# Kernel tuning notes

Hardware: AMD Instinct MI355X
Metric: run time of the kernel (lower is better)

## Reference

```python
import jax, jax.numpy as jnp
import numpy as np

HQ = 32      # query heads
HKV = 8      # kv heads
DH = 128     # head dim
B, S, D = 8, 1, 4096
MAX_SEQ = 4096


def rope(x, pos):
    """Rotary embedding on interleaved pairs. x: [B,S,H,dh], pos: [S] int."""
    d = x.shape[-1]
    theta = 1.0 / (10000.0 ** (jnp.arange(0, d, 2, dtype=jnp.float32) / d))  # [d/2]
    ang = pos[:, None].astype(jnp.float32) * theta[None, :]                  # [S,d/2]
    cos = jnp.cos(ang)[None, :, None, :]
    sin = jnp.sin(ang)[None, :, None, :]
    xr, xi = x[..., 0::2], x[..., 1::2]
    out_r = xr * cos - xi * sin
    out_i = xr * sin + xi * cos
    return jnp.stack([out_r, out_i], axis=-1).reshape(x.shape)


def setup_inputs() -> dict:
    key = jax.random.key(0)
    ks = jax.random.split(key, 8)
    s = 0.02
    return {
        "x": jax.random.normal(ks[0], (B, S, D), jnp.float32),
        "wq": jax.random.normal(ks[1], (D, HQ * DH), jnp.float32) * s,
        "bq": jnp.zeros((HQ * DH,), jnp.float32),
        "wk": jax.random.normal(ks[2], (D, HKV * DH), jnp.float32) * s,
        "bk": jnp.zeros((HKV * DH,), jnp.float32),
        "wv": jax.random.normal(ks[3], (D, HKV * DH), jnp.float32) * s,
        "bv": jnp.zeros((HKV * DH,), jnp.float32),
        "wo": jax.random.normal(ks[4], (HQ * DH, D), jnp.float32) * s,
        "bo": jnp.zeros((D,), jnp.float32),
        "cache_k": jax.random.normal(ks[5], (B, MAX_SEQ, HKV, DH), jnp.float32) * 0.5,
        "cache_v": jax.random.normal(ks[6], (B, MAX_SEQ, HKV, DH), jnp.float32) * 0.5,
        "start_pos": MAX_SEQ - S,  # decode step at end of cache
    }


def reference(x, wq, bq, wk, bk, wv, bv, wo, bo, cache_k, cache_v, start_pos):
    b, s, d = x.shape
    n_rep = HQ // HKV
    q = (x @ wq + bq).reshape(b, s, HQ, DH)
    k = (x @ wk + bk).reshape(b, s, HKV, DH)
    v = (x @ wv + bv).reshape(b, s, HKV, DH)
    pos = start_pos + jnp.arange(s)
    q = rope(q, pos)
    k = rope(k, pos)
    # KV-cache scatter write
    cache_k = jax.lax.dynamic_update_slice(cache_k, k, (0, start_pos, 0, 0))
    cache_v = jax.lax.dynamic_update_slice(cache_v, v, (0, start_pos, 0, 0))
    t = start_pos + s  # static (start_pos is a Python int)
    keys = cache_k[:, :t]    # [B,T,HKV,DH]
    values = cache_v[:, :t]
    # repeat_kv: duplicate each kv head n_rep times -> [B,T,HQ,DH]
    keys = jnp.repeat(keys, n_rep, axis=2)
    values = jnp.repeat(values, n_rep, axis=2)
    # naive softmax attention, score matrix materialized
    scores = jnp.einsum("bshd,bthd->bhst", q, keys) * (DH ** -0.5)  # [B,HQ,S,T]
    attn = jax.nn.softmax(scores, axis=-1)
    out = jnp.einsum("bhst,bthd->bshd", attn, values).reshape(b, s, HQ * DH)
    return out @ wo + bo
```

## Files before the change

### kernel.cpp

```cpp
#include <hip/hip_runtime.h>
#include <cmath>

#define NB 8
#define DIM 4096
#define NHQ 32
#define NHKV 8
#define NDH 128
#define MAXSEQ 4096
#define STARTPOS 4095
#define QKV_COLS 6144
#define RCHUNK 64
#define NRC 64
#define SCALE 0.08838834764831845f

__global__ __launch_bounds__(256) void qkv_partial_k(
    const float* __restrict__ x, const float* __restrict__ wq,
    const float* __restrict__ wk, const float* __restrict__ wv,
    float* __restrict__ part) {
  int bid = blockIdx.x;
  int ct = bid % 12, rc = bid / 12;
  int tid = threadIdx.x;
  const float* W; int ldw; int colbase;
  int gcolbase = ct * 512;
  if (ct < 8)       { W = wq; ldw = NHQ * NDH;  colbase = gcolbase; }
  else if (ct < 10) { W = wk; ldw = NHKV * NDH; colbase = gcolbase - 4096; }
  else              { W = wv; ldw = NHKV * NDH; colbase = gcolbase - 5120; }

  __shared__ __align__(16) float xs[RCHUNK][8];
  int rbase = rc * RCHUNK;
  for (int i = tid; i < RCHUNK * 8; i += 256) {
    int b = i >> 6, r = i & 63;
    xs[r][b] = x[b * DIM + rbase + r];
  }
  __syncthreads();

  int col = colbase + tid * 2;
  const float* wp = W + (size_t)rbase * ldw + col;
  float2 acc[8];
#pragma unroll
  for (int b = 0; b < 8; b++) { acc[b].x = 0.f; acc[b].y = 0.f; }

#pragma unroll 8
  for (int r = 0; r < RCHUNK; r++) {
    float2 w2 = *(const float2*)wp; wp += ldw;
    float4 xa = *(const float4*)&xs[r][0];
    float4 xb = *(const float4*)&xs[r][4];
    acc[0].x += xa.x * w2.x; acc[0].y += xa.x * w2.y;
    acc[1].x += xa.y * w2.x; acc[1].y += xa.y * w2.y;
    acc[2].x += xa.z * w2.x; acc[2].y += xa.z * w2.y;
    acc[3].x += xa.w * w2.x; acc[3].y += xa.w * w2.y;
    acc[4].x += xb.x * w2.x; acc[4].y += xb.x * w2.y;
    acc[5].x += xb.y * w2.x; acc[5].y += xb.y * w2.y;
    acc[6].x += xb.z * w2.x; acc[6].y += xb.z * w2.y;
    acc[7].x += xb.w * w2.x; acc[7].y += xb.w * w2.y;
  }
  int gcol = gcolbase + tid * 2;
#pragma unroll
  for (int b = 0; b < 8; b++)
    *(float2*)&part[((size_t)rc * 8 + b) * QKV_COLS + gcol] = acc[b];
}

__global__ __launch_bounds__(256) void qkv_reduce_rope_k(
    const float* __restrict__ part, const float* __restrict__ bq,
    const float* __restrict__ bk, const float* __restrict__ bv,
    float* __restrict__ qws, float* __restrict__ kws, float* __restrict__ vws) {
  int idx = blockIdx.x * 256 + threadIdx.x;
  int b = idx / QKV_COLS, col = idx % QKV_COLS;
  float s = 0.f;
#pragma unroll 8
  for (int rcc = 0; rcc < NRC; rcc++)
    s += part[((size_t)rcc * 8 + b) * QKV_COLS + col];
  float bias = (col < 4096) ? bq[col] : (col < 5120 ? bk[col - 4096] : bv[col - 5120]);
  s += bias;
  float outv = s;
  if (col < 5120) {
    int dim = col & 127;
    int i2 = dim & ~1;
    float theta = powf(10000.f, -(float)i2 * (1.f / 128.f));
    float ang = (float)STARTPOS * theta;
    float c = cosf(ang), sn = sinf(ang);
    float other = __shfl_xor(s, 1);
    if ((col & 1) == 0) outv = s * c - other * sn;
    else                outv = other * sn + s * c;
  }
  if (col < 4096)       qws[b * 4096 + col] = outv;
  else if (col < 5120)  kws[b * 1024 + (col - 4096)] = outv;
  else                  vws[b * 1024 + (col - 5120)] = outv;
}

__global__ __launch_bounds__(256) void attn_partial_k(
    const float* __restrict__ q, const float* __restrict__ kws,
    const float* __restrict__ vws, const float* __restrict__ ck,
    const float* __restrict__ cv, float* __restrict__ pm,
    float* __restrict__ pl, float* __restrict__ pacc) {
  int bid = blockIdx.x;
  int chunk = bid & 15, grp = bid >> 4;
  int b = grp >> 3, hkv = grp & 7;
  int tid = threadIdx.x;

  __shared__ __align__(16) float kbuf[64][132];
  __shared__ float sbuf[4][256];
  __shared__ __align__(16) float qbuf[4][132];

  for (int i = tid; i < 512; i += 256) {
    int r = i >> 7, d = i & 127;
    qbuf[r][d] = q[b * 4096 + (hkv * 4 + r) * NDH + d];
  }
  __syncthreads();

  int tchunk = chunk * 256;
  int tl_c = tid >> 2;
  int hh = tid & 3;

  for (int tile = 0; tile < 4; tile++) {
    int tbase = tchunk + tile * 64;
#pragma unroll
    for (int i = tid; i < 64 * 32; i += 256) {
      int row = i >> 5, c4 = i & 31;
      int t = tbase + row;
      const float* src = (t == STARTPOS)
          ? (kws + ((size_t)b * NHKV + hkv) * NDH)
          : (ck + (((size_t)b * MAXSEQ + t) * NHKV + hkv) * NDH);
      *(float4*)&kbuf[row][c4 * 4] = *(const float4*)(src + c4 * 4);
    }
    __syncthreads();
    float s0 = 0.f, s1 = 0.f;
    const float4* krow = (const float4*)&kbuf[tl_c][0];
    const float4* qrow = (const float4*)&qbuf[hh][0];
#pragma unroll
    for (int c = 0; c < 32; c += 2) {
      float4 kv = krow[c];     float4 qv = qrow[c];
      s0 += kv.x * qv.x + kv.y * qv.y + kv.z * qv.z + kv.w * qv.w;
      float4 kv2 = krow[c + 1]; float4 qv2 = qrow[c + 1];
      s1 += kv2.x * qv2.x + kv2.y * qv2.y + kv2.z * qv2.z + kv2.w * qv2.w;
    }
    sbuf[hh][tile * 64 + tl_c] = (s0 + s1) * SCALE;
    __syncthreads();
  }

  int wv_ = tid >> 6;
  int lane = tid & 63;
  float e0 = sbuf[wv_][lane];
  float e1 = sbuf[wv_][lane + 64];
  float e2 = sbuf[wv_][lane + 128];
  float e3 = sbuf[wv_][lane + 192];
  float m = fmaxf(fmaxf(e0, e1), fmaxf(e2, e3));
#pragma unroll
  for (int off = 32; off; off >>= 1) m = fmaxf(m, __shfl_xor(m, off));
  float p0 = expf(e0 - m), p1 = expf(e1 - m), p2 = expf(e2 - m), p3 = expf(e3 - m);
  float l = p0 + p1 + p2 + p3;
#pragma unroll
  for (int off = 32; off; off >>= 1) l += __shfl_xor(l, off);
  sbuf[wv_][lane] = p0;
  sbuf[wv_][lane + 64] = p1;
  sbuf[wv_][lane + 128] = p2;
  sbuf[wv_][lane + 192] = p3;
  if (lane == 0) {
    pm[((size_t)grp * 16 + chunk) * 4 + wv_] = m;
    pl[((size_t)grp * 16 + chunk) * 4 + wv_] = l;
  }
  __syncthreads();

  float2 acc2 = {0.f, 0.f};
  int d0 = lane * 2;
  for (int tile = 0; tile < 4; tile++) {
    int tbase = tchunk + tile * 64;
#pragma unroll
    for (int i = tid; i < 64 * 32; i += 256) {
      int row = i >> 5, c4 = i & 31;
      int t = tbase + row;
      const float* src = (t == STARTPOS)
          ? (vws + ((size_t)b * NHKV + hkv) * NDH)
          : (cv + (((size_t)b * MAXSEQ + t) * NHKV + hkv) * NDH);
      *(float4*)&kbuf[row][c4 * 4] = *(const float4*)(src + c4 * 4);
    }
    __syncthreads();
#pragma unroll 8
    for (int tl = 0; tl < 64; tl++) {
      float p = sbuf[wv_][tile * 64 + tl];
      float2 v2 = *(const float2*)&kbuf[tl][d0];
      acc2.x += p * v2.x;
      acc2.y += p * v2.y;
    }
    __syncthreads();
  }
  *(float2*)&pacc[(((size_t)grp * 16 + chunk) * 4 + wv_) * NDH + d0] = acc2;
}

__global__ __launch_bounds__(128) void attn_combine_k(
    const float* __restrict__ pm, const float* __restrict__ pl,
    const float* __restrict__ pacc, float* __restrict__ aout) {
  int bid = blockIdx.x;
  int b = bid >> 5, hq = bid & 31;
  int grp = b * 8 + (hq >> 2), r = hq & 3;
  int d = threadIdx.x;
  float mv[16];
  float M = -1e30f;
#pragma unroll
  for (int c = 0; c < 16; c++) {
    mv[c] = pm[((size_t)grp * 16 + c) * 4 + r];
    M = fmaxf(M, mv[c]);
  }
  float L = 0.f;
  float w[16];
#pragma unroll
  for (int c = 0; c < 16; c++) {
    w[c] = expf(mv[c] - M);
    L += w[c] * pl[((size_t)grp * 16 + c) * 4 + r];
  }
  float o = 0.f;
#pragma unroll
  for (int c = 0; c < 16; c++)
    o += w[c] * pacc[(((size_t)grp * 16 + c) * 4 + r) * NDH + d];
  aout[(size_t)b * 4096 + hq * NDH + d] = o / L;
}

__global__ __launch_bounds__(256) void out_partial_k(
    const float* __restrict__ ain, const float* __restrict__ wo,
    float* __restrict__ part) {
  int bid = blockIdx.x;
  int ct = bid & 7, rc = bid >> 3;
  int tid = threadIdx.x;
  __shared__ __align__(16) float xs[RCHUNK][8];
  int rbase = rc * RCHUNK;
  for (int i = tid; i < RCHUNK * 8; i += 256) {
    int b = i >> 6, r = i & 63;
    xs[r][b] = ain[(size_t)b * 4096 + rbase + r];
  }
  __syncthreads();

  int col = ct * 512 + tid * 2;
  const float* wp = wo + (size_t)rbase * 4096 + col;
  float2 acc[8];
#pragma unroll
  for (int b = 0; b < 8; b++) { acc[b].x = 0.f; acc[b].y = 0.f; }
#pragma unroll 8
  for (int r = 0; r < RCHUNK; r++) {
    float2 w2 = *(const float2*)wp; wp += 4096;
    float4 xa = *(const float4*)&xs[r][0];
    float4 xb = *(const float4*)&xs[r][4];
    acc[0].x += xa.x * w2.x; acc[0].y += xa.x * w2.y;
    acc[1].x += xa.y * w2.x; acc[1].y += xa.y * w2.y;
    acc[2].x += xa.z * w2.x; acc[2].y += xa.z * w2.y;
    acc[3].x += xa.w * w2.x; acc[3].y += xa.w * w2.y;
    acc[4].x += xb.x * w2.x; acc[4].y += xb.x * w2.y;
    acc[5].x += xb.y * w2.x; acc[5].y += xb.y * w2.y;
    acc[6].x += xb.z * w2.x; acc[6].y += xb.z * w2.y;
    acc[7].x += xb.w * w2.x; acc[7].y += xb.w * w2.y;
  }
#pragma unroll
  for (int b = 0; b < 8; b++)
    *(float2*)&part[((size_t)rc * 8 + b) * 4096 + col] = acc[b];
}

__global__ __launch_bounds__(256) void out_reduce_k(
    const float* __restrict__ part, const float* __restrict__ bo,
    float* __restrict__ out) {
  int idx = blockIdx.x * 256 + threadIdx.x;
  int b = idx >> 12, col = idx & 4095;
  float s = bo[col];
#pragma unroll 8
  for (int rcc = 0; rcc < NRC; rcc++)
    s += part[((size_t)rcc * 8 + b) * 4096 + col];
  out[idx] = s;
  (void)b;
}

extern "C" void kernel_launch(void* const* d_in, const int* in_sizes, int n_in,
                              void* d_out, int out_size, void* d_ws, size_t ws_size,
                              hipStream_t stream) {
  const float* x       = (const float*)d_in[0];
  const float* wq      = (const float*)d_in[1];
  const float* bq      = (const float*)d_in[2];
  const float* wk      = (const float*)d_in[3];
  const float* bk      = (const float*)d_in[4];
  const float* wv      = (const float*)d_in[5];
  const float* bv      = (const float*)d_in[6];
  const float* wo      = (const float*)d_in[7];
  const float* bo      = (const float*)d_in[8];
  const float* cache_k = (const float*)d_in[9];
  const float* cache_v = (const float*)d_in[10];
  float* out = (float*)d_out;

  float* ws = (float*)d_ws;
  float* qkv_part = ws;
  float* wo_part  = ws;
  float* qws  = ws + 3145728;
  float* kws  = qws + 32768;
  float* vws  = kws + 8192;
  float* pm   = vws + 8192;
  float* pl   = pm + 4096;
  float* pacc = pl + 4096;
  float* aout = pacc + 524288;

  qkv_partial_k<<<768, 256, 0, stream>>>(x, wq, wk, wv, qkv_part);
  qkv_reduce_rope_k<<<192, 256, 0, stream>>>(qkv_part, bq, bk, bv, qws, kws, vws);
  attn_partial_k<<<1024, 256, 0, stream>>>(qws, kws, vws, cache_k, cache_v, pm, pl, pacc);
  attn_combine_k<<<256, 128, 0, stream>>>(pm, pl, pacc, aout);
  out_partial_k<<<512, 256, 0, stream>>>(aout, wo, wo_part);
  out_reduce_k<<<128, 256, 0, stream>>>(wo_part, bo, out);
}
```

Baseline: 109.1 us.

## Drop LDS staging in attention partial kernel; read K/V rows directly from global

The QK score phase now has each thread compute four head scores for one key row. It streams the row straight from global memory and reads q from global instead of shared memory. The PV phase has each wave read V rows directly with float4 loads, splitting rows between two half-waves and combining them with a shuffle. This removes the shared-memory K/V tiles and most __syncthreads barriers. In exchange, K loads are strided per thread (each lane reads a different 4KB-strided row), and V rows are re-read by all four waves, relying on cache.

```diff
diff --git a/kernel.cpp b/kernel.cpp
--- a/kernel.cpp
+++ b/kernel.cpp
@@ -97,49 +97,38 @@
   int chunk = bid & 15, grp = bid >> 4;
   int b = grp >> 3, hkv = grp & 7;
   int tid = threadIdx.x;
-
-  __shared__ __align__(16) float kbuf[64][132];
+  int wv_ = tid >> 6, lane = tid & 63;
+
   __shared__ float sbuf[4][256];
-  __shared__ __align__(16) float qbuf[4][132];
-
-  for (int i = tid; i < 512; i += 256) {
-    int r = i >> 7, d = i & 127;
-    qbuf[r][d] = q[b * 4096 + (hkv * 4 + r) * NDH + d];
+
+  int tchunk = chunk * 256;
+
+  {
+    int t = tchunk + tid;
+    const float* kr = (t == STARTPOS)
+        ? (kws + ((size_t)b * NHKV + hkv) * NDH)
+        : (ck + (((size_t)b * MAXSEQ + t) * NHKV + hkv) * NDH);
+    const float* qg = q + ((size_t)b * NHQ + hkv * 4) * NDH;
+    float a0 = 0.f, a1 = 0.f, a2 = 0.f, a3 = 0.f;
+#pragma unroll 8
+    for (int j = 0; j < 32; j++) {
+      float4 kv = *(const float4*)(kr + 4 * j);
+      float4 q0 = *(const float4*)(qg + 4 * j);
+      float4 q1 = *(const float4*)(qg + 128 + 4 * j);
+      float4 q2 = *(const float4*)(qg + 256 + 4 * j);
+      float4 q3 = *(const float4*)(qg + 384 + 4 * j);
+      a0 += kv.x * q0.x + kv.y * q0.y + kv.z * q0.z + kv.w * q0.w;
+      a1 += kv.x * q1.x + kv.y * q1.y + kv.z * q1.z + kv.w * q1.w;
+      a2 += kv.x * q2.x + kv.y * q2.y + kv.z * q2.z + kv.w * q2.w;
+      a3 += kv.x * q3.x + kv.y * q3.y + kv.z * q3.z + kv.w * q3.w;
+    }
+    sbuf[0][tid] = a0 * SCALE;
+    sbuf[1][tid] = a1 * SCALE;
+    sbuf[2][tid] = a2 * SCALE;
+    sbuf[3][tid] = a3 * SCALE;
   }
   __syncthreads();
 
-  int tchunk = chunk * 256;
-  int tl_c = tid >> 2;
-  int hh = tid & 3;
-
-  for (int tile = 0; tile < 4; tile++) {
-    int tbase = tchunk + tile * 64;
-#pragma unroll
-    for (int i = tid; i < 64 * 32; i += 256) {
-      int row = i >> 5, c4 = i & 31;
-      int t = tbase + row;
-      const float* src = (t == STARTPOS)
-          ? (kws + ((size_t)b * NHKV + hkv) * NDH)
-          : (ck + (((size_t)b * MAXSEQ + t) * NHKV + hkv) * NDH);
-      *(float4*)&kbuf[row][c4 * 4] = *(const float4*)(src + c4 * 4);
-    }
-    __syncthreads();
-    float s0 = 0.f, s1 = 0.f;
-    const float4* krow = (const float4*)&kbuf[tl_c][0];
-    const float4* qrow = (const float4*)&qbuf[hh][0];
-#pragma unroll
-    for (int c = 0; c < 32; c += 2) {
-      float4 kv = krow[c];     float4 qv = qrow[c];
-      s0 += kv.x * qv.x + kv.y * qv.y + kv.z * qv.z + kv.w * qv.w;
-      float4 kv2 = krow[c + 1]; float4 qv2 = qrow[c + 1];
-      s1 += kv2.x * qv2.x + kv2.y * qv2.y + kv2.z * qv2.z + kv2.w * qv2.w;
-    }
-    sbuf[hh][tile * 64 + tl_c] = (s0 + s1) * SCALE;
-    __syncthreads();
-  }
-
-  int wv_ = tid >> 6;
-  int lane = tid & 63;
   float e0 = sbuf[wv_][lane];
   float e1 = sbuf[wv_][lane + 64];
   float e2 = sbuf[wv_][lane + 128];
@@ -159,32 +148,33 @@
     pm[((size_t)grp * 16 + chunk) * 4 + wv_] = m;
     pl[((size_t)grp * 16 + chunk) * 4 + wv_] = l;
   }
-  __syncthreads();
-
-  float2 acc2 = {0.f, 0.f};
-  int d0 = lane * 2;
-  for (int tile = 0; tile < 4; tile++) {
-    int tbase = tchunk + tile * 64;
-#pragma unroll
-    for (int i = tid; i < 64 * 32; i += 256) {
-      int row = i >> 5, c4 = i & 31;
-      int t = tbase + row;
-      const float* src = (t == STARTPOS)
+
+  int half = lane >> 5;
+  int dq = (lane & 31) * 4;
+  float4 acc = {0.f, 0.f, 0.f, 0.f};
+  const float* vb = cv + (((size_t)b * MAXSEQ + tchunk) * NHKV + hkv) * NDH;
+  for (int tt = 0; tt < 256; tt += 16) {
+#pragma unroll
+    for (int u = 0; u < 8; u++) {
+      int tl = tt + u * 2 + half;
+      int tg = tchunk + tl;
+      const float* vr = (tg == STARTPOS)
           ? (vws + ((size_t)b * NHKV + hkv) * NDH)
-          : (cv + (((size_t)b * MAXSEQ + t) * NHKV + hkv) * NDH);
-      *(float4*)&kbuf[row][c4 * 4] = *(const float4*)(src + c4 * 4);
+          : (vb + (size_t)tl * (NHKV * NDH));
+      float4 v4 = *(const float4*)(vr + dq);
+      float p = sbuf[wv_][tl];
+      acc.x += p * v4.x;
+      acc.y += p * v4.y;
+      acc.z += p * v4.z;
+      acc.w += p * v4.w;
     }
-    __syncthreads();
-#pragma unroll 8
-    for (int tl = 0; tl < 64; tl++) {
-      float p = sbuf[wv_][tile * 64 + tl];
-      float2 v2 = *(const float2*)&kbuf[tl][d0];
-      acc2.x += p * v2.x;
-      acc2.y += p * v2.y;
-    }
-    __syncthreads();
-  }
-  *(float2*)&pacc[(((size_t)grp * 16 + chunk) * 4 + wv_) * NDH + d0] = acc2;
+  }
+  acc.x += __shfl_xor(acc.x, 32);
+  acc.y += __shfl_xor(acc.y, 32);
+  acc.z += __shfl_xor(acc.z, 32);
+  acc.w += __shfl_xor(acc.w, 32);
+  if (half == 0)
+    *(float4*)&pacc[(((size_t)grp * 16 + chunk) * 4 + wv_) * NDH + dq] = acc;
 }
 
 __global__ __launch_bounds__(128) void attn_combine_k(
```

After: 112.9 us. 3.5% more time.

## Split attention into per-batch scores and PV kernels with register-resident queries

Applied to the files above, without the earlier changes.

Replaces the fused per-(batch, kv-head) attention kernel with a scores kernel that covers all 8 kv heads of a batch per block. It keeps the queries in registers, reads K rows directly with double-buffered register loads, and keeps a running online-softmax max and sum per chunk. A separate PV kernel merges the global softmax statistics, normalizes the stored scores into probabilities, and accumulates V with register tiles, followed by a chunk reduction kernel. The aim is fully coalesced streaming of the whole KV row per timestep and no shared-memory staging of K/V. In exchange, the score matrix makes a round trip through global memory and a third kernel launch is added.

```diff
diff --git a/kernel.cpp b/kernel.cpp
--- a/kernel.cpp
+++ b/kernel.cpp
@@ -12,6 +12,8 @@
 #define RCHUNK 64
 #define NRC 64
 #define SCALE 0.08838834764831845f
+
+#define DOT4(k, qq) ((k).x*(qq).x + (k).y*(qq).y + (k).z*(qq).z + (k).w*(qq).w)
 
 __global__ __launch_bounds__(256) void qkv_partial_k(
     const float* __restrict__ x, const float* __restrict__ wq,
@@ -88,131 +90,222 @@
   else                  vws[b * 1024 + (col - 5120)] = outv;
 }
 
-__global__ __launch_bounds__(256) void attn_partial_k(
-    const float* __restrict__ q, const float* __restrict__ kws,
-    const float* __restrict__ vws, const float* __restrict__ ck,
-    const float* __restrict__ cv, float* __restrict__ pm,
-    float* __restrict__ pl, float* __restrict__ pacc) {
+__global__ __launch_bounds__(256, 3) void scores_k(
+    const float* __restrict__ qws, const float* __restrict__ kws,
+    const float* __restrict__ ck, float* __restrict__ S,
+    float* __restrict__ pmx, float* __restrict__ psm) {
   int bid = blockIdx.x;
-  int chunk = bid & 15, grp = bid >> 4;
-  int b = grp >> 3, hkv = grp & 7;
+  int chunk = bid & 127, b = bid >> 7;
   int tid = threadIdx.x;
-
-  __shared__ __align__(16) float kbuf[64][132];
-  __shared__ float sbuf[4][256];
-  __shared__ __align__(16) float qbuf[4][132];
-
-  for (int i = tid; i < 512; i += 256) {
-    int r = i >> 7, d = i & 127;
-    qbuf[r][d] = q[b * 4096 + (hkv * 4 + r) * NDH + d];
-  }
-  __syncthreads();
-
-  int tchunk = chunk * 256;
-  int tl_c = tid >> 2;
-  int hh = tid & 3;
-
-  for (int tile = 0; tile < 4; tile++) {
-    int tbase = tchunk + tile * 64;
-#pragma unroll
-    for (int i = tid; i < 64 * 32; i += 256) {
-      int row = i >> 5, c4 = i & 31;
-      int t = tbase + row;
-      const float* src = (t == STARTPOS)
-          ? (kws + ((size_t)b * NHKV + hkv) * NDH)
-          : (ck + (((size_t)b * MAXSEQ + t) * NHKV + hkv) * NDH);
-      *(float4*)&kbuf[row][c4 * 4] = *(const float4*)(src + c4 * 4);
+  int w = tid >> 6, lane = tid & 63;
+  int p8 = lane >> 3, l8 = lane & 7;
+
+  float4 qf[4][4];
+  const float* qb = qws + ((size_t)b * NHQ + p8 * 4) * NDH + l8 * 4;
+#pragma unroll
+  for (int h = 0; h < 4; h++)
+#pragma unroll
+    for (int j = 0; j < 4; j++)
+      qf[h][j] = *(const float4*)(qb + h * NDH + j * 32);
+
+  const float* kbase = ck + (size_t)(b * MAXSEQ + chunk * 32) * (NHKV * NDH);
+  const float* kwsrow = kws + ((size_t)b * NHKV + p8) * NDH + l8 * 4;
+
+  float m_run = -1e30f, s_run = 0.f;
+  float4 ka[4], kb_[4];
+
+#define SLOAD(buf, i_) { \
+    const float* kr_; \
+    if (chunk * 32 + (i_) * 4 + w == STARTPOS) kr_ = kwsrow; \
+    else kr_ = kbase + (size_t)((i_) * 32 + w * 8 + p8) * NDH + l8 * 4; \
+    buf[0] = *(const float4*)(kr_);       buf[1] = *(const float4*)(kr_ + 32); \
+    buf[2] = *(const float4*)(kr_ + 64);  buf[3] = *(const float4*)(kr_ + 96); }
+
+#define SPROC(buf, i_) { \
+    float a0 = DOT4(buf[0],qf[0][0])+DOT4(buf[1],qf[0][1])+DOT4(buf[2],qf[0][2])+DOT4(buf[3],qf[0][3]); \
+    float a1 = DOT4(buf[0],qf[1][0])+DOT4(buf[1],qf[1][1])+DOT4(buf[2],qf[1][2])+DOT4(buf[3],qf[1][3]); \
+    float a2 = DOT4(buf[0],qf[2][0])+DOT4(buf[1],qf[2][1])+DOT4(buf[2],qf[2][2])+DOT4(buf[3],qf[2][3]); \
+    float a3 = DOT4(buf[0],qf[3][0])+DOT4(buf[1],qf[3][1])+DOT4(buf[2],qf[3][2])+DOT4(buf[3],qf[3][3]); \
+    a0 += __shfl_xor(a0,1); a0 += __shfl_xor(a0,2); a0 += __shfl_xor(a0,4); \
+    a1 += __shfl_xor(a1,1); a1 += __shfl_xor(a1,2); a1 += __shfl_xor(a1,4); \
+    a2 += __shfl_xor(a2,1); a2 += __shfl_xor(a2,2); a2 += __shfl_xor(a2,4); \
+    a3 += __shfl_xor(a3,1); a3 += __shfl_xor(a3,2); a3 += __shfl_xor(a3,4); \
+    float v_ = ((l8==0)?a0:(l8==1)?a1:(l8==2)?a2:a3) * SCALE; \
+    int tg_ = chunk * 32 + (i_) * 4 + w; \
+    if (l8 < 4) S[((size_t)b * MAXSEQ + tg_) * NHQ + p8 * 4 + l8] = v_; \
+    float mn_ = fmaxf(m_run, v_); \
+    s_run = s_run * expf(m_run - mn_) + expf(v_ - mn_); \
+    m_run = mn_; }
+
+  SLOAD(ka, 0); SLOAD(kb_, 1);
+  SPROC(ka, 0); SLOAD(ka, 2);
+  SPROC(kb_, 1); SLOAD(kb_, 3);
+  SPROC(ka, 2); SLOAD(ka, 4);
+  SPROC(kb_, 3); SLOAD(kb_, 5);
+  SPROC(ka, 4); SLOAD(ka, 6);
+  SPROC(kb_, 5); SLOAD(kb_, 7);
+  SPROC(ka, 6);
+  SPROC(kb_, 7);
+#undef SLOAD
+#undef SPROC
+
+  __shared__ float red[4][NHQ][2];
+  if (l8 < 4) { red[w][p8 * 4 + l8][0] = m_run; red[w][p8 * 4 + l8][1] = s_run; }
+  __syncthreads();
+  if (tid < NHQ) {
+    float M = red[0][tid][0], L = red[0][tid][1];
+#pragma unroll
+    for (int ww = 1; ww < 4; ww++) {
+      float m2 = red[ww][tid][0], l2 = red[ww][tid][1];
+      float Mn = fmaxf(M, m2);
+      L = L * expf(M - Mn) + l2 * expf(m2 - Mn);
+      M = Mn;
+    }
+    pmx[((size_t)b * 128 + chunk) * NHQ + tid] = M;
+    psm[((size_t)b * 128 + chunk) * NHQ + tid] = L;
+  }
+}
+
+__global__ __launch_bounds__(256, 2) void pv_k(
+    const float* __restrict__ S, const float* __restrict__ pmx,
+    const float* __restrict__ psm, const float* __restrict__ vws,
+    const float* __restrict__ cv, float* __restrict__ pacc) {
+  int bid = blockIdx.x;
+  int chunk = bid & 63, b = bid >> 6;
+  int tid = threadIdx.x;
+  int w = tid >> 6, lane = tid & 63;
+  int p8 = lane >> 3, l8 = lane & 7;
+
+  __shared__ float ml[NHQ][2];
+  __shared__ float pbuf[NHQ][65];
+  __shared__ float red2[8][NHQ][2];
+  __shared__ __align__(16) float axl[3][64][68];
+
+  {
+    int hq = tid & 31, part = tid >> 5;
+    float M = -1e30f, L = 0.f;
+    for (int c = part; c < 128; c += 8) {
+      float m2 = pmx[((size_t)b * 128 + c) * NHQ + hq];
+      float l2 = psm[((size_t)b * 128 + c) * NHQ + hq];
+      float Mn = fmaxf(M, m2);
+      L = L * expf(M - Mn) + l2 * expf(m2 - Mn);
+      M = Mn;
+    }
+    red2[part][hq][0] = M; red2[part][hq][1] = L;
+    __syncthreads();
+    if (tid < NHQ) {
+      float M0 = red2[0][tid][0], L0 = red2[0][tid][1];
+#pragma unroll
+      for (int pp = 1; pp < 8; pp++) {
+        float m2 = red2[pp][tid][0], l2 = red2[pp][tid][1];
+        float Mn = fmaxf(M0, m2);
+        L0 = L0 * expf(M0 - Mn) + l2 * expf(m2 - Mn);
+        M0 = Mn;
+      }
+      ml[tid][0] = M0; ml[tid][1] = 1.0f / L0;
     }
     __syncthreads();
-    float s0 = 0.f, s1 = 0.f;
-    const float4* krow = (const float4*)&kbuf[tl_c][0];
-    const float4* qrow = (const float4*)&qbuf[hh][0];
-#pragma unroll
-    for (int c = 0; c < 32; c += 2) {
-      float4 kv = krow[c];     float4 qv = qrow[c];
-      s0 += kv.x * qv.x + kv.y * qv.y + kv.z * qv.z + kv.w * qv.w;
-      float4 kv2 = krow[c + 1]; float4 qv2 = qrow[c + 1];
-      s1 += kv2.x * qv2.x + kv2.y * qv2.y + kv2.z * qv2.z + kv2.w * qv2.w;
-    }
-    sbuf[hh][tile * 64 + tl_c] = (s0 + s1) * SCALE;
-    __syncthreads();
-  }
-
-  int wv_ = tid >> 6;
-  int lane = tid & 63;
-  float e0 = sbuf[wv_][lane];
-  float e1 = sbuf[wv_][lane + 64];
-  float e2 = sbuf[wv_][lane + 128];
-  float e3 = sbuf[wv_][lane + 192];
-  float m = fmaxf(fmaxf(e0, e1), fmaxf(e2, e3));
-#pragma unroll
-  for (int off = 32; off; off >>= 1) m = fmaxf(m, __shfl_xor(m, off));
-  float p0 = expf(e0 - m), p1 = expf(e1 - m), p2 = expf(e2 - m), p3 = expf(e3 - m);
-  float l = p0 + p1 + p2 + p3;
-#pragma unroll
-  for (int off = 32; off; off >>= 1) l += __shfl_xor(l, off);
-  sbuf[wv_][lane] = p0;
-  sbuf[wv_][lane + 64] = p1;
-  sbuf[wv_][lane + 128] = p2;
-  sbuf[wv_][lane + 192] = p3;
-  if (lane == 0) {
-    pm[((size_t)grp * 16 + chunk) * 4 + wv_] = m;
-    pl[((size_t)grp * 16 + chunk) * 4 + wv_] = l;
-  }
-  __syncthreads();
-
-  float2 acc2 = {0.f, 0.f};
-  int d0 = lane * 2;
-  for (int tile = 0; tile < 4; tile++) {
-    int tbase = tchunk + tile * 64;
-#pragma unroll
-    for (int i = tid; i < 64 * 32; i += 256) {
-      int row = i >> 5, c4 = i & 31;
-      int t = tbase + row;
-      const float* src = (t == STARTPOS)
-          ? (vws + ((size_t)b * NHKV + hkv) * NDH)
-          : (cv + (((size_t)b * MAXSEQ + t) * NHKV + hkv) * NDH);
-      *(float4*)&kbuf[row][c4 * 4] = *(const float4*)(src + c4 * 4);
-    }
-    __syncthreads();
-#pragma unroll 8
-    for (int tl = 0; tl < 64; tl++) {
-      float p = sbuf[wv_][tile * 64 + tl];
-      float2 v2 = *(const float2*)&kbuf[tl][d0];
-      acc2.x += p * v2.x;
-      acc2.y += p * v2.y;
-    }
-    __syncthreads();
-  }
-  *(float2*)&pacc[(((size_t)grp * 16 + chunk) * 4 + wv_) * NDH + d0] = acc2;
-}
-
-__global__ __launch_bounds__(128) void attn_combine_k(
-    const float* __restrict__ pm, const float* __restrict__ pl,
+  }
+
+  for (int idx = tid; idx < 64 * NHQ; idx += 256) {
+    int tl = idx >> 5, hq = idx & 31;
+    float s = S[((size_t)b * MAXSEQ + chunk * 64 + tl) * NHQ + hq];
+    pbuf[hq][tl] = expf(s - ml[hq][0]) * ml[hq][1];
+  }
+  __syncthreads();
+
+  const float* vbase = cv + (size_t)(b * MAXSEQ + chunk * 64) * (NHKV * NDH);
+  const float* vwsrow = vws + ((size_t)b * NHKV + p8) * NDH + l8 * 4;
+
+  float4 acc[4][4];
+#pragma unroll
+  for (int h = 0; h < 4; h++)
+#pragma unroll
+    for (int j = 0; j < 4; j++) acc[h][j] = (float4){0.f, 0.f, 0.f, 0.f};
+
+  float4 va[4], vb_[4];
+
+#define VLOAD(buf, i_) { \
+    const float* vr_; \
+    if (chunk * 64 + (i_) * 4 + w == STARTPOS) vr_ = vwsrow; \
+    else vr_ = vbase + (size_t)((i_) * 32 + w * 8 + p8) * NDH + l8 * 4; \
+    buf[0] = *(const float4*)(vr_);       buf[1] = *(const float4*)(vr_ + 32); \
+    buf[2] = *(const float4*)(vr_ + 64);  buf[3] = *(const float4*)(vr_ + 96); }
+
+#define VPROC(buf, i_) { \
+    int tl_ = (i_) * 4 + w; \
+    float pp0 = pbuf[p8 * 4 + 0][tl_]; \
+    float pp1 = pbuf[p8 * 4 + 1][tl_]; \
+    float pp2 = pbuf[p8 * 4 + 2][tl_]; \
+    float pp3 = pbuf[p8 * 4 + 3][tl_]; \
+    _Pragma("unroll") \
+    for (int j = 0; j < 4; j++) { \
+      acc[0][j].x += pp0 * buf[j].x; acc[0][j].y += pp0 * buf[j].y; \
+      acc[0][j].z += pp0 * buf[j].z; acc[0][j].w += pp0 * buf[j].w; \
+      acc[1][j].x += pp1 * buf[j].x; acc[1][j].y += pp1 * buf[j].y; \
+      acc[1][j].z += pp1 * buf[j].z; acc[1][j].w += pp1 * buf[j].w; \
+      acc[2][j].x += pp2 * buf[j].x; acc[2][j].y += pp2 * buf[j].y; \
+      acc[2][j].z += pp2 * buf[j].z; acc[2][j].w += pp2 * buf[j].w; \
+      acc[3][j].x += pp3 * buf[j].x; acc[3][j].y += pp3 * buf[j].y; \
+      acc[3][j].z += pp3 * buf[j].z; acc[3][j].w += pp3 * buf[j].w; } }
+
+  VLOAD(va, 0); VLOAD(vb_, 1);
+  VPROC(va, 0);  VLOAD(va, 2);
+  VPROC(vb_, 1); VLOAD(vb_, 3);
+  VPROC(va, 2);  VLOAD(va, 4);
+  VPROC(vb_, 3); VLOAD(vb_, 5);
+  VPROC(va, 4);  VLOAD(va, 6);
+  VPROC(vb_, 5); VLOAD(vb_, 7);
+  VPROC(va, 6);  VLOAD(va, 8);
+  VPROC(vb_, 7); VLOAD(vb_, 9);
+  VPROC(va, 8);  VLOAD(va, 10);
+  VPROC(vb_, 9); VLOAD(vb_, 11);
+  VPROC(va, 10); VLOAD(va, 12);
+  VPROC(vb_, 11); VLOAD(vb_, 13);
+  VPROC(va, 12); VLOAD(va, 14);
+  VPROC(vb_, 13); VLOAD(vb_, 15);
+  VPROC(va, 14);
+  VPROC(vb_, 15);
+#undef VLOAD
+#undef VPROC
+
+  if (w > 0) {
+#pragma unroll
+    for (int h = 0; h < 4; h++)
+#pragma unroll
+      for (int j = 0; j < 4; j++)
+        *(float4*)&axl[w - 1][lane][h * 16 + j * 4] = acc[h][j];
+  }
+  __syncthreads();
+  if (w == 0) {
+#pragma unroll
+    for (int ww = 0; ww < 3; ww++)
+#pragma unroll
+      for (int h = 0; h < 4; h++)
+#pragma unroll
+        for (int j = 0; j < 4; j++) {
+          float4 t4 = *(const float4*)&axl[ww][lane][h * 16 + j * 4];
+          acc[h][j].x += t4.x; acc[h][j].y += t4.y;
+          acc[h][j].z += t4.z; acc[h][j].w += t4.w;
+        }
+    float* pb = pacc + (((size_t)chunk * NB + b) * NHQ + p8 * 4) * NDH + l8 * 4;
+#pragma unroll
+    for (int h = 0; h < 4; h++)
+#pragma unroll
+      for (int j = 0; j < 4; j++)
+        *(float4*)(pb + h * NDH + j * 32) = acc[h][j];
+  }
+}
+
+__global__ __launch_bounds__(256) void pv_reduce_k(
     const float* __restrict__ pacc, float* __restrict__ aout) {
-  int bid = blockIdx.x;
-  int b = bid >> 5, hq = bid & 31;
-  int grp = b * 8 + (hq >> 2), r = hq & 3;
-  int d = threadIdx.x;
-  float mv[16];
-  float M = -1e30f;
-#pragma unroll
-  for (int c = 0; c < 16; c++) {
-    mv[c] = pm[((size_t)grp * 16 + c) * 4 + r];
-    M = fmaxf(M, mv[c]);
-  }
-  float L = 0.f;
-  float w[16];
-#pragma unroll
-  for (int c = 0; c < 16; c++) {
-    w[c] = expf(mv[c] - M);
-    L += w[c] * pl[((size_t)grp * 16 + c) * 4 + r];
-  }
-  float o = 0.f;
-#pragma unroll
-  for (int c = 0; c < 16; c++)
-    o += w[c] * pacc[(((size_t)grp * 16 + c) * 4 + r) * NDH + d];
-  aout[(size_t)b * 4096 + hq * NDH + d] = o / L;
+  int idx = blockIdx.x * 256 + threadIdx.x;
+  int b = idx >> 12, rest = idx & 4095;
+  float s = 0.f;
+#pragma unroll 8
+  for (int c = 0; c < 64; c++)
+    s += pacc[((size_t)c * NB + b) * 4096 + rest];
+  aout[idx] = s;
 }
 
 __global__ __launch_bounds__(256) void out_partial_k(
@@ -284,19 +377,21 @@
 
   float* ws = (float*)d_ws;
   float* qkv_part = ws;
+  float* pacc     = ws;
   float* wo_part  = ws;
-  float* qws  = ws + 3145728;
-  float* kws  = qws + 32768;
-  float* vws  = kws + 8192;
-  float* pm   = vws + 8192;
-  float* pl   = pm + 4096;
-  float* pacc = pl + 4096;
-  float* aout = pacc + 524288;
+  float* pmx  = ws + 2097152;
+  float* psm  = ws + 2097152 + 32768;
+  float* S    = ws + 3145728;
+  float* qws  = ws + 4194304;
+  float* kws  = ws + 4227072;
+  float* vws  = ws + 4235264;
+  float* aout = ws + 4243456;
 
   qkv_partial_k<<<768, 256, 0, stream>>>(x, wq, wk, wv, qkv_part);
   qkv_reduce_rope_k<<<192, 256, 0, stream>>>(qkv_part, bq, bk, bv, qws, kws, vws);
-  attn_partial_k<<<1024, 256, 0, stream>>>(qws, kws, vws, cache_k, cache_v, pm, pl, pacc);
-  attn_combine_k<<<256, 128, 0, stream>>>(pm, pl, pacc, aout);
+  scores_k<<<1024, 256, 0, stream>>>(qws, kws, cache_k, S, pmx, psm);
+  pv_k<<<512, 256, 0, stream>>>(S, pmx, psm, vws, cache_v, pacc);
+  pv_reduce_k<<<128, 256, 0, stream>>>(pacc, aout);
   out_partial_k<<<512, 256, 0, stream>>>(aout, wo, wo_part);
   out_reduce_k<<<128, 256, 0, stream>>>(wo_part, bo, out);
 }
```

Result: slower. 118.6 us (+8.7%).
